# Kernel tuning notes

Hardware: AMD Instinct MI355X
Metric: run time of the kernel (lower is better)

## Reference

```python
import jax, jax.numpy as jnp
import numpy as np

B, C_IN, F, N = 32, 512, 128, 16   # batch, in_channels, frame_n, node_n
C_OUT, K = 512, 2                  # out_channels, per-node upsample kernel width


def setup_inputs() -> dict:
    key = jax.random.key(0)
    k1, k2, k3 = jax.random.split(key, 3)
    x = jax.random.normal(k1, (B, C_IN, F, N), dtype=jnp.float32)
    # Stacked ConvTranspose2d weights: torch layout [C_in, C_out, 1, K] per node,
    # stacked over nodes -> [N, C_in, C_out, K]. Per-node bias -> [N, C_out].
    W = jax.random.normal(k2, (N, C_IN, C_OUT, K), dtype=jnp.float32) * 0.02
    b = jax.random.normal(k3, (N, C_OUT), dtype=jnp.float32) * 0.02
    return {"x": x, "W": W, "b": b}


def reference(x, W, b):
    # Per-node ConvTranspose2d(C_in, C_out, (1,K)) on a width-1 input is a linear
    # expansion: y[b,o,f,n,k] = sum_c x[b,c,f,n] * W[n,c,o,k] + bias[n,o].
    y = jnp.einsum('bcfn,ncok->bofnk', x, W) + b.T[None, :, None, :, None]
    Bs, O, Fs, Ns, Ks = y.shape
    y1 = y.reshape(Bs, O, Fs, Ns * Ks)  # concat over nodes along last dim
    # Index-scatter reassembly: out[..., index[i]] = y1[..., i].
    # Flattened samplelist = [0,1,...,N*K-1] (identity), so this is a no-op
    # (matching the torch aliasing semantics exactly for identity permutation).
    index = jnp.arange(Ns * Ks)
    out = y1.at[:, :, :, index].set(y1)
    return out
```

## Files before the change

kernel.cpp:

```cpp
#include <hip/hip_runtime.h>


typedef unsigned short u16;
typedef unsigned int u32;
typedef __attribute__((ext_vector_type(8))) u16 u16x8;
typedef __attribute__((ext_vector_type(8))) __bf16 bf16x8;
typedef __attribute__((ext_vector_type(4))) float f32x4;

typedef const __attribute__((address_space(1))) void* gas_p;
typedef __attribute__((address_space(3))) void* las_p;

__device__ __forceinline__ u16 f2bf(float f) {
    u32 u = __float_as_uint(f);
    u += 0x7fffu + ((u >> 16) & 1u);
    return (u16)(u >> 16);
}
__device__ __forceinline__ float bf2f(u32 lo16) {
    return __uint_as_float(lo16 << 16);
}
__device__ __forceinline__ void g2l16(const void* g, void* l) {
    __builtin_amdgcn_global_load_lds((gas_p)g, (las_p)l, 16, 0, 0);
}

__global__ __launch_bounds__(256) void k_transpose_x(const float* __restrict__ x,
                                                     u16* __restrict__ xT) {
    int bid = blockIdx.x;
    int ct  = bid & 7;
    int ftl = (bid >> 3) & 7;
    int b   = bid >> 6;
    int c0 = ct * 64, f0 = ftl * 16;
    int t = threadIdx.x;
    int fi = t >> 4, n = t & 15;
    const float* xb = x + (size_t)b * 1048576 + (size_t)f0 * 16 + t;
    u16* dst = xT + ((size_t)n * 4096 + b * 128 + f0 + fi) * 512 + c0;
#pragma unroll
    for (int c8 = 0; c8 < 8; ++c8) {
        u16x8 v;
#pragma unroll
        for (int e = 0; e < 8; ++e)
            v[e] = f2bf(xb[(size_t)(c0 + c8 * 8 + e) * 2048]);
        *(u16x8*)&dst[c8 * 8] = v;
    }
}

__global__ __launch_bounds__(256) void k_transpose_w(const float* __restrict__ W,
                                                     u16* __restrict__ WbT) {
    int v = blockIdx.x * 256 + threadIdx.x;
    int j  = v & 1023;
    int c8 = (v >> 10) & 63;
    int n  = v >> 16;
    const float* src = W + (size_t)n * 524288 + (size_t)c8 * 8192 + j;
    u16x8 o;
#pragma unroll
    for (int e = 0; e < 8; ++e)
        o[e] = f2bf(src[(size_t)e * 1024]);
    *(u16x8*)&WbT[((size_t)n * 1024 + j) * 512 + c8 * 8] = o;
}

__global__ __launch_bounds__(256) void k_gemm(const u16* __restrict__ xT,
                                              const u16* __restrict__ WbT,
                                              const float* __restrict__ bias,
                                              u16* __restrict__ Y) {
    int bid = blockIdx.x;
    int jt = bid & 7;
    int mt = (bid >> 3) & 31;
    int n  = bid >> 8;
    int m0 = mt * 128, j0 = jt * 128;
    int t = threadIdx.x;
    int w = t >> 6, l = t & 63;
    int wr = w >> 1, wc = w & 1;

    __shared__ __align__(16) u16 As[128][32];
    __shared__ __align__(16) u16 Bs[128][32];

    const u16* An = xT  + ((size_t)n * 4096 + m0) * 512;
    const u16* Bn = WbT + ((size_t)n * 1024 + j0) * 512;

    int row_a = t >> 2;
    int coff  = (t & 3) * 8;
    char* AsB = (char*)&As[0][0];
    char* BsB = (char*)&Bs[0][0];

    f32x4 acc[4][4] = {};

    for (int kt = 0; kt < 16; ++kt) {
        int c0 = kt * 32;
        g2l16(&An[(size_t)row_a * 512 + c0 + coff],        AsB + t * 16);
        g2l16(&An[(size_t)(row_a + 64) * 512 + c0 + coff], AsB + 4096 + t * 16);
        g2l16(&Bn[(size_t)row_a * 512 + c0 + coff],        BsB + t * 16);
        g2l16(&Bn[(size_t)(row_a + 64) * 512 + c0 + coff], BsB + 4096 + t * 16);
        asm volatile("s_waitcnt vmcnt(0)" ::: "memory");
        __syncthreads();

        bf16x8 a[4], bb[4];
#pragma unroll
        for (int mi = 0; mi < 4; ++mi)
            a[mi] = *(const bf16x8*)&As[wr * 64 + mi * 16 + (l & 15)][(l >> 4) * 8];
#pragma unroll
        for (int ji = 0; ji < 4; ++ji)
            bb[ji] = *(const bf16x8*)&Bs[wc * 64 + ji * 16 + (l & 15)][(l >> 4) * 8];
#pragma unroll
        for (int mi = 0; mi < 4; ++mi)
#pragma unroll
            for (int ji = 0; ji < 4; ++ji)
                acc[mi][ji] = __builtin_amdgcn_mfma_f32_16x16x32_bf16(
                    a[mi], bb[ji], acc[mi][ji], 0, 0, 0);
        __syncthreads();
    }

    float bv[4];
#pragma unroll
    for (int ji = 0; ji < 4; ++ji) {
        int j = j0 + wc * 64 + ji * 16 + (l & 15);
        bv[ji] = bias[n * 512 + (j >> 1)];
    }
    u16* Yn = Y + (size_t)n * 4194304;
#pragma unroll
    for (int mi = 0; mi < 4; ++mi) {
        int rbase = m0 + wr * 64 + mi * 16 + (l >> 4) * 4;
#pragma unroll
        for (int r = 0; r < 4; ++r) {
            int m = rbase + r;
#pragma unroll
            for (int ji = 0; ji < 4; ++ji) {
                int j = j0 + wc * 64 + ji * 16 + (l & 15);
                Yn[(size_t)m * 1024 + j] = f2bf(acc[mi][ji][r] + bv[ji]);
            }
        }
    }
}

__global__ __launch_bounds__(256) void k_reassemble(const u16* __restrict__ Y,
                                                    float* __restrict__ out) {
    int bid = blockIdx.x;
    int ft = bid & 7;
    int ot = (bid >> 3) & 31;
    int b  = bid >> 8;
    int f0 = ft * 16, o0 = ot * 16;
    int t = threadIdx.x;

    __shared__ __align__(16) unsigned char st[16 * 1296];
    {
        int n = t >> 4, fi = t & 15;
        const u16* src = Y + ((size_t)n * 4096 + b * 128 + f0 + fi) * 1024 + o0 * 2;
        u16x8* dst = (u16x8*)&st[n * 1296 + fi * 80];
        const u16x8* s8 = (const u16x8*)src;
        dst[0] = s8[0]; dst[1] = s8[1]; dst[2] = s8[2]; dst[3] = s8[3];
    }
    __syncthreads();

    float* ob = out + (size_t)b * 2097152 + (size_t)o0 * 4096 + (size_t)f0 * 32;
#pragma unroll
    for (int i = 0; i < 8; ++i) {
        int w4  = i * 256 + t;
        int o_l = w4 >> 7;
        int fi  = (w4 >> 3) & 15;
        int nk4 = w4 & 7;
        int n0  = nk4 * 2;
        u32 p0 = *(const u32*)&st[n0 * 1296 + fi * 80 + o_l * 4];
        u32 p1 = *(const u32*)&st[(n0 + 1) * 1296 + fi * 80 + o_l * 4];
        float4 v;
        v.x = bf2f(p0 & 0xffffu); v.y = bf2f(p0 >> 16);
        v.z = bf2f(p1 & 0xffffu); v.w = bf2f(p1 >> 16);
        *(float4*)&ob[(size_t)o_l * 4096 + fi * 32 + nk4 * 4] = v;
    }
}

__global__ __launch_bounds__(256) void k_fallback(const float* __restrict__ x,
                                                  const float* __restrict__ W,
                                                  const float* __restrict__ bias,
                                                  float* __restrict__ out) {
    int bid = blockIdx.x;
    int jt = bid & 15;
    int mt = (bid >> 4) & 63;
    int n  = bid >> 10;
    int m0 = mt * 64;
    int b  = m0 >> 7;
    int f0 = m0 & 127;
    int j0 = jt * 64;
    int t = threadIdx.x;
    int tr = t >> 4, tc = t & 15;
    __shared__ float xs[16][65];
    __shared__ float wt[16][65];
    float acc[4][4] = {};
    const float* xb = x + (size_t)b * 1048576 + (size_t)f0 * 16 + n;
    const float* Wn = W + (size_t)n * 524288 + j0;
    for (int c0 = 0; c0 < 512; c0 += 16) {
#pragma unroll
        for (int i = 0; i < 4; ++i) {
            int v  = i * 256 + t;
            int ci = v >> 6, e = v & 63;
            xs[ci][e] = xb[(size_t)(c0 + ci) * 2048 + (size_t)e * 16];
            wt[ci][e] = Wn[(size_t)(c0 + ci) * 1024 + e];
        }
        __syncthreads();
#pragma unroll
        for (int c = 0; c < 16; ++c) {
            float a0 = xs[c][tr * 4], a1 = xs[c][tr * 4 + 1],
                  a2 = xs[c][tr * 4 + 2], a3 = xs[c][tr * 4 + 3];
            float w0 = wt[c][tc * 4], w1 = wt[c][tc * 4 + 1],
                  w2 = wt[c][tc * 4 + 2], w3 = wt[c][tc * 4 + 3];
            acc[0][0] = fmaf(a0, w0, acc[0][0]); acc[0][1] = fmaf(a0, w1, acc[0][1]);
            acc[0][2] = fmaf(a0, w2, acc[0][2]); acc[0][3] = fmaf(a0, w3, acc[0][3]);
            acc[1][0] = fmaf(a1, w0, acc[1][0]); acc[1][1] = fmaf(a1, w1, acc[1][1]);
            acc[1][2] = fmaf(a1, w2, acc[1][2]); acc[1][3] = fmaf(a1, w3, acc[1][3]);
            acc[2][0] = fmaf(a2, w0, acc[2][0]); acc[2][1] = fmaf(a2, w1, acc[2][1]);
            acc[2][2] = fmaf(a2, w2, acc[2][2]); acc[2][3] = fmaf(a2, w3, acc[2][3]);
            acc[3][0] = fmaf(a3, w0, acc[3][0]); acc[3][1] = fmaf(a3, w1, acc[3][1]);
            acc[3][2] = fmaf(a3, w2, acc[3][2]); acc[3][3] = fmaf(a3, w3, acc[3][3]);
        }
        __syncthreads();
    }
#pragma unroll
    for (int r = 0; r < 4; ++r) {
        int f = f0 + tr * 4 + r;
#pragma unroll
        for (int q = 0; q < 4; ++q) {
            int j = j0 + tc * 4 + q;
            int o = j >> 1, k = j & 1;
            out[(size_t)b * 2097152 + (size_t)o * 4096 + (size_t)f * 32 + n * 2 + k] =
                acc[r][q] + bias[n * 512 + o];
        }
    }
}

extern "C" void kernel_launch(void* const* d_in, const int* in_sizes, int n_in,
                              void* d_out, int out_size, void* d_ws, size_t ws_size,
                              hipStream_t stream) {
    (void)in_sizes; (void)n_in; (void)out_size;
    const float* x    = (const float*)d_in[0];
    const float* W    = (const float*)d_in[1];
    const float* bias = (const float*)d_in[2];
    float* out = (float*)d_out;

    const size_t xT_bytes = 67108864;
    const size_t Wb_bytes = 16777216;
    const size_t Y_bytes  = 134217728;
    const size_t need = xT_bytes + Wb_bytes + Y_bytes;

    if (ws_size >= need) {
        u16* xT  = (u16*)d_ws;
        u16* WbT = (u16*)((char*)d_ws + xT_bytes);
        u16* Y   = (u16*)((char*)d_ws + xT_bytes + Wb_bytes);
        k_transpose_x<<<dim3(2048), dim3(256), 0, stream>>>(x, xT);
        k_transpose_w<<<dim3(4096), dim3(256), 0, stream>>>(W, WbT);
        k_gemm<<<dim3(4096), dim3(256), 0, stream>>>(xT, WbT, bias, Y);
        k_reassemble<<<dim3(8192), dim3(256), 0, stream>>>(Y, out);
    } else {
        k_fallback<<<dim3(16384), dim3(256), 0, stream>>>(x, W, bias, out);
    }
}
```

Baseline: 593.4 us.

## Stage bf16 transposes through swizzled LDS and remap GEMM blocks per XCD

Both transpose kernels now write converted bf16 vectors into a swizzled shared-memory tile and then write them out as contiguous 128-byte row segments. This replaces the earlier scattered 16-byte global stores. The W transpose is retiled into 64x256 blocks, so it launches fewer, larger blocks. The GEMM block index is remapped so that each XCD handles a fixed set of nodes, which is meant to improve L2 reuse of the per-node weight and input tiles. The changes add LDS traffic and a barrier in the transposes.

```diff
diff --git a/kernel.cpp b/kernel.cpp
--- a/kernel.cpp
+++ b/kernel.cpp
@@ -30,41 +30,70 @@
     int b   = bid >> 6;
     int c0 = ct * 64, f0 = ftl * 16;
     int t = threadIdx.x;
-    int fi = t >> 4, n = t & 15;
-    const float* xb = x + (size_t)b * 1048576 + (size_t)f0 * 16 + t;
-    u16* dst = xT + ((size_t)n * 4096 + b * 128 + f0 + fi) * 512 + c0;
+    const float* xb = x + (size_t)b * 1048576 + (size_t)c0 * 2048 + f0 * 16 + t;
+
+    __shared__ __align__(16) u16x8 st[256][8];
+
 #pragma unroll
     for (int c8 = 0; c8 < 8; ++c8) {
         u16x8 v;
 #pragma unroll
         for (int e = 0; e < 8; ++e)
-            v[e] = f2bf(xb[(size_t)(c0 + c8 * 8 + e) * 2048]);
-        *(u16x8*)&dst[c8 * 8] = v;
+            v[e] = f2bf(xb[(size_t)(c8 * 8 + e) * 2048]);
+        st[t][c8 ^ (t & 7)] = v;
+    }
+    __syncthreads();
+#pragma unroll
+    for (int it = 0; it < 8; ++it) {
+        int rr = it * 32 + (t >> 3);
+        int ch = t & 7;
+        u16x8 v = st[rr][ch ^ (rr & 7)];
+        u16* dst = xT + ((size_t)(rr & 15) * 4096 + b * 128 + f0 + (rr >> 4)) * 512
+                      + c0 + ch * 8;
+        *(u16x8*)dst = v;
     }
 }
 
 __global__ __launch_bounds__(256) void k_transpose_w(const float* __restrict__ W,
                                                      u16* __restrict__ WbT) {
-    int v = blockIdx.x * 256 + threadIdx.x;
-    int j  = v & 1023;
-    int c8 = (v >> 10) & 63;
-    int n  = v >> 16;
-    const float* src = W + (size_t)n * 524288 + (size_t)c8 * 8192 + j;
-    u16x8 o;
-#pragma unroll
-    for (int e = 0; e < 8; ++e)
-        o[e] = f2bf(src[(size_t)e * 1024]);
-    *(u16x8*)&WbT[((size_t)n * 1024 + j) * 512 + c8 * 8] = o;
+    int bid = blockIdx.x;
+    int ct = bid & 7;
+    int jt = (bid >> 3) & 3;
+    int n  = bid >> 5;
+    int c0 = ct * 64, j0 = jt * 256;
+    int t = threadIdx.x;
+    const float* src = W + (size_t)n * 524288 + (size_t)c0 * 1024 + j0 + t;
+
+    __shared__ __align__(16) u16x8 st[256][8];
+
+#pragma unroll
+    for (int c8 = 0; c8 < 8; ++c8) {
+        u16x8 v;
+#pragma unroll
+        for (int e = 0; e < 8; ++e)
+            v[e] = f2bf(src[(size_t)(c8 * 8 + e) * 1024]);
+        st[t][c8 ^ (t & 7)] = v;
+    }
+    __syncthreads();
+#pragma unroll
+    for (int it = 0; it < 8; ++it) {
+        int rr = it * 32 + (t >> 3);
+        int ch = t & 7;
+        u16x8 v = st[rr][ch ^ (rr & 7)];
+        *(u16x8*)&WbT[((size_t)n * 1024 + j0 + rr) * 512 + c0 + ch * 8] = v;
+    }
 }
 
 __global__ __launch_bounds__(256) void k_gemm(const u16* __restrict__ xT,
                                               const u16* __restrict__ WbT,
                                               const float* __restrict__ bias,
                                               u16* __restrict__ Y) {
-    int bid = blockIdx.x;
-    int jt = bid & 7;
-    int mt = (bid >> 3) & 31;
-    int n  = bid >> 8;
+    int p = blockIdx.x;
+    int xcd = p & 7;
+    int s   = p >> 3;
+    int jt  = s & 7;
+    int mt  = (s >> 3) & 31;
+    int n   = xcd + ((s >> 8) << 3);
     int m0 = mt * 128, j0 = jt * 128;
     int t = threadIdx.x;
     int w = t >> 6, l = t & 63;
@@ -243,7 +272,7 @@
         u16* WbT = (u16*)((char*)d_ws + xT_bytes);
         u16* Y   = (u16*)((char*)d_ws + xT_bytes + Wb_bytes);
         k_transpose_x<<<dim3(2048), dim3(256), 0, stream>>>(x, xT);
-        k_transpose_w<<<dim3(4096), dim3(256), 0, stream>>>(W, WbT);
+        k_transpose_w<<<dim3(512), dim3(256), 0, stream>>>(W, WbT);
         k_gemm<<<dim3(4096), dim3(256), 0, stream>>>(xT, WbT, bias, Y);
         k_reassemble<<<dim3(8192), dim3(256), 0, stream>>>(Y, out);
     } else {
```

After: 520.8 us. 1.14x faster.
